# Kernel tuning notes

Measured on AMD Instinct MI355X. Metric: run time of the kernel, lower is better.

The kernel has to match this reference:

```python
import jax, jax.numpy as jnp
import numpy as np

# ---- fixed constants from stft2hcfp.__init__ ----
FS = 16000.0; FR = 2.0; FC = 27.5; TC = 1.0 / 4487.0; NPO = 48
N = int(FS / FR)                      # 8000 FFT length
HALF_N = int(round(N / 2))            # 4000
SQRT_N = float(np.sqrt(N))
HIGH_FREQ_IDX = int(round(1.0 / TC / FR) + 1)   # 2245
HIGH_QUEF_IDX = int(round(FS / FC)) + 1         # 583
CUT_Q = int(round(FS * TC))           # 4  (cepstrum cutoff)
TOTAL_BINS = 4 * 88                   # 352 log-freq bins
NUM_HARMONIC = 5

def _central_freqs():
    stop = 1.0 / TC
    nest = int(np.ceil(np.log2(stop / FC)) * NPO)
    cf = []
    for i in range(nest):
        c = FC * 2.0 ** (float(i) / NPO)
        if c < stop:
            cf.append(c)
        else:
            break
    return cf

CF = _central_freqs()   # 353 central frequencies
NEST = len(CF)

def _freq_matrix():
    # triangular log-frequency filterbank over linear freq axis
    f = (FS * np.linspace(0, 0.5, HALF_N, endpoint=True))[:HIGH_FREQ_IDX]
    W = np.zeros((NEST - 1, len(f)), np.float32)
    for i in range(1, NEST - 1):
        l = int(round(CF[i - 1] / FR)); r = int(round(CF[i + 1] / FR) + 1)
        if l >= r - 1:
            W[i, l] = 1.0
        else:
            for j in range(l, r):
                if CF[i - 1] < f[j] < CF[i]:
                    W[i, j] = (f[j] - CF[i - 1]) / (CF[i] - CF[i - 1])
                elif CF[i] < f[j] < CF[i + 1]:
                    W[i, j] = (CF[i + 1] - f[j]) / (CF[i + 1] - CF[i])
    return W

def _quef_matrix():
    q = np.arange(HIGH_QUEF_IDX) / FS + 1e-6
    fq = 1.0 / q
    W = np.zeros((NEST - 1, len(fq)), np.float32)
    for i in range(1, NEST - 1):
        for j in range(int(round(FS / CF[i + 1])), int(round(FS / CF[i - 1]) + 1)):
            if j >= len(fq):
                continue
            if CF[i - 1] < fq[j] < CF[i]:
                W[i, j] = (fq[j] - CF[i - 1]) / (CF[i] - CF[i - 1])
            elif CF[i] < fq[j] < CF[i + 1]:
                W[i, j] = (CF[i + 1] - fq[j]) / (CF[i + 1] - CF[i])
    return W

# harmonic shift indices: closest central freq to (k+1)*27.5 Hz, k=0..5
HIDS = [int(np.argmin(np.abs(np.asarray(CF) - (k + 1) * FC))) for k in range(NUM_HARMONIC + 1)]


def _nonlinear(x, g, cutoff):
    # relu + pow(g), then zero first/last `cutoff` rows along axis 1.
    # safe pow: grad is 0 where x<=0 (matches relu-masked torch behavior, no inf at 0)
    y = jnp.where(x > 0, jnp.where(x > 0, x, 1.0) ** g, 0.0)
    y = y.at[:, :cutoff].set(0.0).at[:, -cutoff:].set(0.0)
    return y


def setup_inputs() -> dict:
    key = jax.random.key(0)
    dx = jax.random.uniform(key, (8, 512, N), dtype=jnp.float32)  # [B, T, 8000] spectrogram
    return {
        "dx": dx,
        "W_freq": jnp.asarray(_freq_matrix()),   # [352, 2245]
        "W_quef": jnp.asarray(_quef_matrix()),   # [352, 583]
    }


def reference(dx, W_freq, W_quef):
    tfr0 = jnp.swapaxes(dx, 1, 2)                       # [B, F=8000, T]
    # CFP layer 1: real part of FFT over freq axis -> cepstrum, nonlinear g=0.6
    ceps = jnp.fft.fft(tfr0, axis=1).real / SQRT_N      # [B, 8000, T]
    ceps = _nonlinear(ceps, 0.6, CUT_Q)
    # log-frequency mappings (banded triangular filterbanks)
    tfr0h = tfr0[:, :HIGH_FREQ_IDX]                      # [B, 2245, T]
    cepsh = ceps[:, :HIGH_QUEF_IDX]                      # [B, 583, T]
    tfrL0 = jnp.einsum('kf,bft->bkt', W_freq, tfr0h)     # [B, 352, T]
    tfrLQ = jnp.einsum('kq,bqt->bkt', W_quef, cepsh)     # [B, 352, T]
    # harmonic stacking: shift down (spectral) / shift up (cepstral)
    har_s = [jnp.pad(tfrL0[:, h:TOTAL_BINS], ((0, 0), (0, h), (0, 0))) for h in HIDS]
    har_c = [jnp.pad(tfrLQ[:, :TOTAL_BINS - h], ((0, 0), (h, 0), (0, 0))) for h in HIDS]
    piece = jnp.concatenate([jnp.stack(har_s, axis=1), jnp.stack(har_c, axis=1)], axis=1)
    return jnp.swapaxes(piece, 2, 3)                     # [B, 12, T, 352]
```

## Files before the change

### kernel.cpp

```cpp
#include <hip/hip_runtime.h>
#include <hip/hip_bf16.h>
#include <limits.h>

typedef __attribute__((ext_vector_type(8))) short short8;
typedef __attribute__((ext_vector_type(4))) float f32x4;
typedef __attribute__((ext_vector_type(16))) float f32x16;

#define NN 8000
#define NCOL 4096
#define KBINS 352
#define QPAD 640
#define QH 320
#define BN 256
#define KC 8
#define NTILE 64
#define KSTEP 8
#define CUTQ 4
#define T_ 512
#define WFB 64
#define WQB 20
#define LTS 528

#define GLL16(g, l) __builtin_amdgcn_global_load_lds( \
    (const __attribute__((address_space(1))) unsigned int*)(g), \
    (__attribute__((address_space(3))) unsigned int*)(l), 16, 0, 0)

static __device__ __forceinline__ ushort bfc(float f){
  __hip_bfloat16 h = __float2bfloat16(f);
  return *reinterpret_cast<ushort*>(&h);
}
static __device__ __forceinline__ float b2f(ushort u){
  unsigned v = ((unsigned)u) << 16; float f; __builtin_memcpy(&f, &v, 4); return f;
}

__global__ void gen_cos_k(ushort* __restrict__ cosg, int HQI){
  int n = blockIdx.x*256 + threadIdx.x;
  int q = blockIdx.y;
  float v = 0.f;
  if (q < HQI){
    int m = (q*n) % NN;
    v = cosf((float)m * 7.8539816339744831e-4f);
  }
  int kt = n >> 6, s8 = (n >> 3) & 7, e = n & 7;
  cosg[(size_t)kt*(QPAD*64) + (size_t)q*64 + (((s8 ^ (q & 7)) << 3) | e)] = bfc(v);
}

__global__ __launch_bounds__(512, 2) void fold_k(const float* __restrict__ dx,
                                                 ushort* __restrict__ xf){
  __shared__ ushort lbuf[NTILE*LTS];
  int rg = blockIdx.x;
  int t = threadIdx.x;
  int w = t >> 6, l = t & 63;
  int row = rg*8 + w;
  const float* rp = dx + (size_t)row*NN;
  int swz = (row & 7) << 3;

  #pragma unroll
  for (int sub=0; sub<8; ++sub){
    int n0 = sub*512 + l*8;
    f32x4 p0 = *(const f32x4*)(rp + n0);
    f32x4 p1 = *(const f32x4*)(rp + n0 + 4);
    f32x4 ma = *(const f32x4*)(rp + 7996 - n0);
    f32x4 mb = *(const f32x4*)(rp + 7992 - n0);
    float ms = rp[n0 ? NN - n0 : 0];
    float pr[8] = {p0[0],p0[1],p0[2],p0[3],p1[0],p1[1],p1[2],p1[3]};
    float mi[8] = {n0 ? ms : 0.f, ma[3],ma[2],ma[1],ma[0],mb[3],mb[2],mb[1]};
    short8 o;
    #pragma unroll
    for (int e=0;e<8;e++){
      int n = n0 + e;
      float v;
      if (n == 0)          v = pr[0];
      else if (n < 4000)   v = pr[e] + mi[e];
      else if (n == 4000)  v = pr[e];
      else                 v = 0.f;
      o[e] = (short)bfc(v);
    }
    int kt = n0 >> 6, s8 = n0 & 56;
    *(short8*)(&lbuf[kt*LTS + w*64 + (s8 ^ swz)]) = o;
  }
  __syncthreads();

  #pragma unroll
  for (int j=0;j<8;++j){
    int kt = j*8 + w;
    short8 v = *(const short8*)(&lbuf[kt*LTS + l*8]);
    *(short8*)(&xf[((size_t)kt*NCOL + rg*8)*64 + l*8]) = v;
  }
}

__global__ void bp_k(const float* __restrict__ Wf, const float* __restrict__ Wq,
                     int HFI, int HQI, int* __restrict__ fLo, int* __restrict__ qLo,
                     float* __restrict__ WfT, float* __restrict__ WqT){
  __shared__ int slo, shi;
  int r = blockIdx.x;
  bool isF = (blockIdx.y == 0);
  const float* W = isF ? Wf : Wq;
  int width = isF ? HFI : HQI;
  int bw    = isF ? WFB : WQB;
  float* WT = isF ? WfT : WqT;
  int* Lo   = isF ? fLo : qLo;
  if (threadIdx.x==0){ slo = INT_MAX; shi = -1; }
  __syncthreads();
  int mylo = INT_MAX, myhi = -1;
  for (int c = threadIdx.x; c < width; c += 256){
    if (W[(size_t)r*width + c] != 0.f){ if (c < mylo) mylo = c; if (c > myhi) myhi = c; }
  }
  atomicMin(&slo, mylo); atomicMax(&shi, myhi);
  __syncthreads();
  int l = (shi < 0) ? 0 : slo, h = (shi < 0) ? 0 : shi + 1;
  if (threadIdx.x==0) Lo[r] = l;
  for (int j = threadIdx.x; j < bw; j += 256){
    float v = 0.f;
    if (l + j < h) v = W[(size_t)r*width + l + j];
    WT[(size_t)j*KBINS + r] = v;
  }
}

__global__ __launch_bounds__(512, 2) void gemm_k(const ushort* __restrict__ xf,
                                                 const ushort* __restrict__ cosg,
                                                 ushort* __restrict__ part){
  __shared__ ushort As[2][QH*64];
  __shared__ ushort Bs[2][BN*64];
  int tid = threadIdx.x;
  int nb = blockIdx.x, qh = blockIdx.y, kc = blockIdx.z;
  int lane = tid & 63, widx = tid >> 6;
  int wm = widx & 1, wn = widx >> 1;
  int l31 = lane & 31, lh = lane >> 5;
  int kt0 = kc*KSTEP, ktE = kt0 + KSTEP;

  const ushort* ag0 = cosg + (size_t)qh*(QH*64) + tid*8;
  const ushort* bg0 = xf + (size_t)nb*(BN*64) + tid*8;

  #define STAGE(kt_, buf_) { \
    const ushort* ag_ = ag0 + (size_t)(kt_)*(QPAD*64); \
    _Pragma("unroll") \
    for (int i_=0;i_<5;i_++) GLL16(ag_ + i_*4096, &As[buf_][tid*8 + i_*4096]); \
    const ushort* bg_ = bg0 + (size_t)(kt_)*(NCOL*64); \
    _Pragma("unroll") \
    for (int i_=0;i_<4;i_++) GLL16(bg_ + i_*4096, &Bs[buf_][tid*8 + i_*4096]); }

  f32x16 acc[5][2];
  #pragma unroll
  for (int a=0;a<5;a++){ acc[a][0] = (f32x16)0.f; acc[a][1] = (f32x16)0.f; }

  STAGE(kt0, 0);

  int cur = 0;
  for (int kt = kt0; kt < ktE; ++kt){
    if (kt + 1 < ktE){
      STAGE(kt+1, cur^1);
      asm volatile("s_waitcnt vmcnt(9)" ::: "memory");
    } else {
      asm volatile("s_waitcnt vmcnt(0)" ::: "memory");
    }
    __builtin_amdgcn_s_barrier();
    __builtin_amdgcn_sched_barrier(0);
    const ushort* Ac = &As[cur][0];
    const ushort* Bc = &Bs[cur][0];
    #pragma unroll
    for (int p=0;p<4;p++){
      short8 dfr[2];
      #pragma unroll
      for (int c=0;c<2;c++){
        int row = wn*64 + c*32 + l31;
        dfr[c] = *(const short8*)(Bc + row*64 + ((((p<<1)|lh) ^ (row & 7)) << 3));
      }
      short8 cfr[5];
      #pragma unroll
      for (int a=0;a<5;a++){
        int row = wm*160 + a*32 + l31;
        cfr[a] = *(const short8*)(Ac + row*64 + ((((p<<1)|lh) ^ (row & 7)) << 3));
      }
      __builtin_amdgcn_s_setprio(1);
      #pragma unroll
      for (int a=0;a<5;a++){
        acc[a][0] = __builtin_amdgcn_mfma_f32_32x32x16_bf16(dfr[0], cfr[a], acc[a][0], 0,0,0);
        acc[a][1] = __builtin_amdgcn_mfma_f32_32x32x16_bf16(dfr[1], cfr[a], acc[a][1], 0,0,0);
      }
      __builtin_amdgcn_s_setprio(0);
      __builtin_amdgcn_sched_barrier(0);
      __builtin_amdgcn_s_barrier();
      __builtin_amdgcn_sched_barrier(0);
    }
    cur ^= 1;
  }

  ushort* pb = part + (size_t)kc*NCOL*QPAD;
  #pragma unroll
  for (int a=0;a<5;a++){
    int q = qh*QH + wm*160 + a*32 + l31;
    #pragma unroll
    for (int c=0;c<2;c++){
      int colb = nb*BN + wn*64 + c*32 + 4*lh;
      #pragma unroll
      for (int r=0;r<16;r++){
        int col = colb + (r&3) + 8*(r>>2);
        pb[(size_t)col*QPAD + q] = bfc(acc[a][c][r]);
      }
    }
  }
}

__global__ __launch_bounds__(384) void fuse_k(const float* __restrict__ dx,
        const ushort* __restrict__ part,
        const float* __restrict__ WfT, const float* __restrict__ WqT,
        const int* __restrict__ fLo, const int* __restrict__ qLo,
        float* __restrict__ out, int HFI, int HQI){
  __shared__ float xr[2368];
  __shared__ float yq[QPAD];
  __shared__ float tl0[KBINS];
  __shared__ float tlq[KBINS];
  int col = blockIdx.x;
  int b = col >> 9, t = col & 511;
  int tid = threadIdx.x;
  const float invs = 0.011180339887498949f;

  for (int f = tid; f < 2368; f += 384) xr[f] = (f < HFI) ? dx[(size_t)col*NN + f] : 0.f;
  const ushort* pc = part + (size_t)col*QPAD;
  for (int q = tid; q < QPAD; q += 384){
    float y = 0.f;
    if (q < HQI){
      float s = 0.f;
      #pragma unroll
      for (int kc=0; kc<KC; kc++) s += b2f(pc[(size_t)kc*NCOL*QPAD + q]);
      s *= invs;
      if (q >= CUTQ && s > 0.f) y = powf(s, 0.6f);
    }
    yq[q] = y;
  }
  __syncthreads();

  if (tid < KBINS){
    int k = tid;
    int lo = fLo[k];
    float aF = 0.f;
    #pragma unroll
    for (int j=0;j<WFB;j++) aF += WfT[j*KBINS + k] * xr[lo + j];
    int ql = qLo[k];
    float aQ = 0.f;
    #pragma unroll
    for (int j=0;j<WQB;j++) aQ += WqT[j*KBINS + k] * yq[ql + j];
    tl0[k] = aF; tlq[k] = aQ;
  }
  __syncthreads();

  const int hids[6] = {0,48,76,96,111,124};
  for (int u = tid; u < 12*KBINS; u += 384){
    int j = u / KBINS;
    int k = u - j*KBINS;
    int h = hids[(j < 6) ? j : j - 6];
    float v;
    if (j < 6) v = (k + h < KBINS) ? tl0[k + h] : 0.f;
    else       v = (k >= h)        ? tlq[k - h] : 0.f;
    out[(((size_t)b*12 + j)*T_ + t)*KBINS + k] = v;
  }
}

extern "C" void kernel_launch(void* const* d_in, const int* in_sizes, int n_in,
                              void* d_out, int out_size, void* d_ws, size_t ws_size,
                              hipStream_t stream){
  const float* dx = (const float*)d_in[0];
  const float* Wf = (const float*)d_in[1];
  const float* Wq = (const float*)d_in[2];
  int HFI = in_sizes[1] / KBINS;
  int HQI = in_sizes[2] / KBINS;
  float* out = (float*)d_out;
  char* ws = (char*)d_ws;

  ushort* cosg = (ushort*)ws;
  size_t off = (size_t)NTILE*QPAD*64*2;
  ushort* xf = (ushort*)(ws + off); off += (size_t)NTILE*NCOL*64*2;
  ushort* part = (ushort*)(ws + off); off += (size_t)KC*NCOL*QPAD*2;
  int* fLo = (int*)(ws+off); off += KBINS*4;
  int* qLo = (int*)(ws+off); off += KBINS*4;
  float* WfT = (float*)(ws+off); off += (size_t)WFB*KBINS*4;
  float* WqT = (float*)(ws+off); off += (size_t)WQB*KBINS*4;
  (void)n_in; (void)out_size; (void)ws_size;

  gen_cos_k<<<dim3(16, QPAD), 256, 0, stream>>>(cosg, HQI);
  fold_k<<<NCOL/8, 512, 0, stream>>>(dx, xf);
  bp_k<<<dim3(KBINS, 2), 256, 0, stream>>>(Wf, Wq, HFI, HQI, fLo, qLo, WfT, WqT);
  gemm_k<<<dim3(NCOL/BN, QPAD/QH, KC), 512, 0, stream>>>(xf, cosg, part);
  fuse_k<<<NCOL, 384, 0, stream>>>(dx, part, WfT, WqT, fLo, qLo, out, HFI, HQI);
}
```

Baseline: 135.5 us.

## Replace symmetric fold with even/odd quefrency split for the cosine GEMM

Uses cos(2πq(n+4000)/N) = (-1)^q·cos(2πqn/N) to split the real DFT into two halves. Even quefrencies multiply x[n]+x[n+4000] and odd ones multiply x[n]-x[n+4000], each against a 320-row cosine table. This replaces the reversed-index fold kernel, which needed LDS staging, with a simple contiguous prep kernel, and remaps the partial-output slots in the fuse step. The GEMM does the same total work, but each parity now reads its own B operand, so the two grid halves no longer share B data through cache.

```diff
diff --git a/kernel.cpp b/kernel.cpp
--- a/kernel.cpp
+++ b/kernel.cpp
@@ -19,7 +19,6 @@
 #define T_ 512
 #define WFB 64
 #define WQB 20
-#define LTS 528
 
 #define GLL16(g, l) __builtin_amdgcn_global_load_lds( \
     (const __attribute__((address_space(1))) unsigned int*)(g), \
@@ -33,60 +32,47 @@
   unsigned v = ((unsigned)u) << 16; float f; __builtin_memcpy(&f, &v, 4); return f;
 }
 
-__global__ void gen_cos_k(ushort* __restrict__ cosg, int HQI){
+__global__ void gen_cos_k(ushort* __restrict__ cosp, int HQI){
   int n = blockIdx.x*256 + threadIdx.x;
-  int q = blockIdx.y;
+  int u = blockIdx.y;
+  int par = blockIdx.z;
+  int q = 2*u + par;
   float v = 0.f;
-  if (q < HQI){
+  if (q < HQI && n < 4000){
     int m = (q*n) % NN;
     v = cosf((float)m * 7.8539816339744831e-4f);
   }
   int kt = n >> 6, s8 = (n >> 3) & 7, e = n & 7;
-  cosg[(size_t)kt*(QPAD*64) + (size_t)q*64 + (((s8 ^ (q & 7)) << 3) | e)] = bfc(v);
-}
-
-__global__ __launch_bounds__(512, 2) void fold_k(const float* __restrict__ dx,
-                                                 ushort* __restrict__ xf){
-  __shared__ ushort lbuf[NTILE*LTS];
-  int rg = blockIdx.x;
-  int t = threadIdx.x;
-  int w = t >> 6, l = t & 63;
-  int row = rg*8 + w;
+  cosp[((size_t)par*NTILE + kt)*(QH*64) + (size_t)u*64 + (((s8 ^ (u & 7)) << 3) | e)] = bfc(v);
+}
+
+__global__ __launch_bounds__(256) void prep_k(const float* __restrict__ dx,
+                                              ushort* __restrict__ xs){
+  int uid = blockIdx.x*256 + threadIdx.x;
+  int row = uid >> 9;
+  int n0 = (uid & 511) * 8;
   const float* rp = dx + (size_t)row*NN;
-  int swz = (row & 7) << 3;
-
-  #pragma unroll
-  for (int sub=0; sub<8; ++sub){
-    int n0 = sub*512 + l*8;
-    f32x4 p0 = *(const f32x4*)(rp + n0);
-    f32x4 p1 = *(const f32x4*)(rp + n0 + 4);
-    f32x4 ma = *(const f32x4*)(rp + 7996 - n0);
-    f32x4 mb = *(const f32x4*)(rp + 7992 - n0);
-    float ms = rp[n0 ? NN - n0 : 0];
-    float pr[8] = {p0[0],p0[1],p0[2],p0[3],p1[0],p1[1],p1[2],p1[3]};
-    float mi[8] = {n0 ? ms : 0.f, ma[3],ma[2],ma[1],ma[0],mb[3],mb[2],mb[1]};
-    short8 o;
-    #pragma unroll
-    for (int e=0;e<8;e++){
-      int n = n0 + e;
-      float v;
-      if (n == 0)          v = pr[0];
-      else if (n < 4000)   v = pr[e] + mi[e];
-      else if (n == 4000)  v = pr[e];
-      else                 v = 0.f;
-      o[e] = (short)bfc(v);
-    }
-    int kt = n0 >> 6, s8 = n0 & 56;
-    *(short8*)(&lbuf[kt*LTS + w*64 + (s8 ^ swz)]) = o;
-  }
-  __syncthreads();
-
-  #pragma unroll
-  for (int j=0;j<8;++j){
-    int kt = j*8 + w;
-    short8 v = *(const short8*)(&lbuf[kt*LTS + l*8]);
-    *(short8*)(&xf[((size_t)kt*NCOL + rg*8)*64 + l*8]) = v;
-  }
+  short8 oe, oo;
+  if (n0 < 4000){
+    f32x4 a0 = *(const f32x4*)(rp + n0);
+    f32x4 a1 = *(const f32x4*)(rp + n0 + 4);
+    f32x4 b0 = *(const f32x4*)(rp + 4000 + n0);
+    f32x4 b1 = *(const f32x4*)(rp + 4004 + n0);
+    #pragma unroll
+    for (int e=0;e<4;e++){
+      oe[e]   = (short)bfc(a0[e] + b0[e]);
+      oo[e]   = (short)bfc(a0[e] - b0[e]);
+      oe[4+e] = (short)bfc(a1[e] + b1[e]);
+      oo[4+e] = (short)bfc(a1[e] - b1[e]);
+    }
+  } else {
+    #pragma unroll
+    for (int e=0;e<8;e++){ oe[e] = 0; oo[e] = 0; }
+  }
+  int kt = n0 >> 6, s8 = (n0 >> 3) & 7;
+  size_t base = ((size_t)kt*NCOL + row)*64 + ((s8 ^ (row & 7)) << 3);
+  *(short8*)(&xs[base]) = oe;
+  *(short8*)(&xs[(size_t)NTILE*NCOL*64 + base]) = oo;
 }
 
 __global__ void bp_k(const float* __restrict__ Wf, const float* __restrict__ Wq,
@@ -117,23 +103,23 @@
   }
 }
 
-__global__ __launch_bounds__(512, 2) void gemm_k(const ushort* __restrict__ xf,
-                                                 const ushort* __restrict__ cosg,
+__global__ __launch_bounds__(512, 2) void gemm_k(const ushort* __restrict__ xs,
+                                                 const ushort* __restrict__ cosp,
                                                  ushort* __restrict__ part){
   __shared__ ushort As[2][QH*64];
   __shared__ ushort Bs[2][BN*64];
   int tid = threadIdx.x;
-  int nb = blockIdx.x, qh = blockIdx.y, kc = blockIdx.z;
+  int nb = blockIdx.x, par = blockIdx.y, kc = blockIdx.z;
   int lane = tid & 63, widx = tid >> 6;
   int wm = widx & 1, wn = widx >> 1;
   int l31 = lane & 31, lh = lane >> 5;
   int kt0 = kc*KSTEP, ktE = kt0 + KSTEP;
 
-  const ushort* ag0 = cosg + (size_t)qh*(QH*64) + tid*8;
-  const ushort* bg0 = xf + (size_t)nb*(BN*64) + tid*8;
+  const ushort* ag0 = cosp + (size_t)par*(NTILE*QH*64) + tid*8;
+  const ushort* bg0 = xs + (size_t)par*(NTILE*NCOL*64) + (size_t)nb*(BN*64) + tid*8;
 
   #define STAGE(kt_, buf_) { \
-    const ushort* ag_ = ag0 + (size_t)(kt_)*(QPAD*64); \
+    const ushort* ag_ = ag0 + (size_t)(kt_)*(QH*64); \
     _Pragma("unroll") \
     for (int i_=0;i_<5;i_++) GLL16(ag_ + i_*4096, &As[buf_][tid*8 + i_*4096]); \
     const ushort* bg_ = bg0 + (size_t)(kt_)*(NCOL*64); \
@@ -189,14 +175,14 @@
   ushort* pb = part + (size_t)kc*NCOL*QPAD;
   #pragma unroll
   for (int a=0;a<5;a++){
-    int q = qh*QH + wm*160 + a*32 + l31;
+    int slot = par*QH + wm*160 + a*32 + l31;
     #pragma unroll
     for (int c=0;c<2;c++){
       int colb = nb*BN + wn*64 + c*32 + 4*lh;
       #pragma unroll
       for (int r=0;r<16;r++){
         int col = colb + (r&3) + 8*(r>>2);
-        pb[(size_t)col*QPAD + q] = bfc(acc[a][c][r]);
+        pb[(size_t)col*QPAD + slot] = bfc(acc[a][c][r]);
       }
     }
   }
@@ -221,9 +207,10 @@
   for (int q = tid; q < QPAD; q += 384){
     float y = 0.f;
     if (q < HQI){
+      int slot = (q & 1)*QH + (q >> 1);
       float s = 0.f;
       #pragma unroll
-      for (int kc=0; kc<KC; kc++) s += b2f(pc[(size_t)kc*NCOL*QPAD + q]);
+      for (int kc=0; kc<KC; kc++) s += b2f(pc[(size_t)kc*NCOL*QPAD + slot]);
       s *= invs;
       if (q >= CUTQ && s > 0.f) y = powf(s, 0.6f);
     }
@@ -268,9 +255,9 @@
   float* out = (float*)d_out;
   char* ws = (char*)d_ws;
 
-  ushort* cosg = (ushort*)ws;
-  size_t off = (size_t)NTILE*QPAD*64*2;
-  ushort* xf = (ushort*)(ws + off); off += (size_t)NTILE*NCOL*64*2;
+  ushort* cosp = (ushort*)ws;
+  size_t off = (size_t)2*NTILE*QH*64*2;
+  ushort* xs = (ushort*)(ws + off); off += (size_t)2*NTILE*NCOL*64*2;
   ushort* part = (ushort*)(ws + off); off += (size_t)KC*NCOL*QPAD*2;
   int* fLo = (int*)(ws+off); off += KBINS*4;
   int* qLo = (int*)(ws+off); off += KBINS*4;
@@ -278,9 +265,9 @@
   float* WqT = (float*)(ws+off); off += (size_t)WQB*KBINS*4;
   (void)n_in; (void)out_size; (void)ws_size;
 
-  gen_cos_k<<<dim3(16, QPAD), 256, 0, stream>>>(cosg, HQI);
-  fold_k<<<NCOL/8, 512, 0, stream>>>(dx, xf);
+  gen_cos_k<<<dim3(16, QH, 2), 256, 0, stream>>>(cosp, HQI);
+  prep_k<<<NCOL*2, 256, 0, stream>>>(dx, xs);
   bp_k<<<dim3(KBINS, 2), 256, 0, stream>>>(Wf, Wq, HFI, HQI, fLo, qLo, WfT, WqT);
-  gemm_k<<<dim3(NCOL/BN, QPAD/QH, KC), 512, 0, stream>>>(xf, cosg, part);
+  gemm_k<<<dim3(NCOL/BN, 2, KC), 512, 0, stream>>>(xs, cosp, part);
   fuse_k<<<NCOL, 384, 0, stream>>>(dx, part, WfT, WqT, fLo, qLo, out, HFI, HQI);
 }
```

After: 141.1 us. 4.1% more time.
